# Performance work log

Measured on AMD Instinct MI355X. Metric: run time of the kernel, lower is better.

## Reference

```python
import jax, jax.numpy as jnp
import numpy as np

NODE_V = 16  # node_vocab_size
EDGE_V = 8   # edge_vocab_size
B, N = 64, 256


def _encode_single(x, vocab_size):
    # round to integer bucket, map bucket centers to (-1, 1)
    return 2.0 * ((jnp.round(x) + 0.5) / vocab_size) - 1.0


def setup_inputs() -> dict:
    key = jax.random.key(0)
    k1, k2, k3 = jax.random.split(key, 3)
    x_nodes = jax.random.uniform(k1, (B, N, 1), dtype=jnp.float32, minval=0.0, maxval=float(NODE_V))
    x_edges = jax.random.uniform(k2, (B, N, N), dtype=jnp.float32, minval=0.0, maxval=float(EDGE_V))
    g_0 = jax.random.normal(k3, (B,), dtype=jnp.float32)
    return {"x_nodes": x_nodes, "x_edges": x_edges, "g_0": g_0}


def reference(x_nodes, x_edges, g_0):
    # encode: quantize continuous inputs to bucket centers in (-1, 1)
    zn = _encode_single(x_nodes, NODE_V)  # [b, n, 1]
    ze = _encode_single(x_edges, EDGE_V)  # [b, n, n]

    # codebook values for each vocab bucket, also mapped to (-1, 1)
    node_vals = _encode_single(jnp.arange(NODE_V, dtype=jnp.float32), NODE_V)  # [Vn]
    edge_vals = _encode_single(jnp.arange(EDGE_V, dtype=jnp.float32), EDGE_V)  # [Ve]

    inv_stdev = jnp.exp(-0.5 * g_0)  # [b]

    # decode nodes: [b, n, 1] - [Vn] -> [b, n, Vn]
    node_logits = -0.5 * jnp.square((zn - node_vals) * inv_stdev[:, None, None])
    node_logprobs = jax.nn.log_softmax(node_logits, axis=-1)

    # decode edges: [b, n, n, 1] - [Ve] -> [b, n, n, Ve]
    edge_logits = -0.5 * jnp.square((ze[..., None] - edge_vals) * inv_stdev[:, None, None, None])
    edge_logprobs = jax.nn.log_softmax(edge_logits, axis=-1)

    return node_logprobs, edge_logprobs
```

## Files before the change

### kernel.cpp

```cpp
#include <hip/hip_runtime.h>
#include <hip/hip_bf16.h>

#define NODE_V 16
#define EDGE_V 8
#define BATCH  64
#define NSEQ   256

__global__ void node_kernel(const float* __restrict__ xn,
                            const float* __restrict__ g0,
                            float* __restrict__ out) {
    __shared__ __align__(16) float tbl[17 * 16];
    const int b = blockIdx.x;

    if (threadIdx.x < 17) {
        const float inv = __expf(-0.5f * g0[b]) ;
        const float inv_acc = expf(-0.5f * g0[b]);
        (void)inv;
        const int bucket = threadIdx.x;
        const float z = 2.0f * ((float)bucket + 0.5f) / (float)NODE_V - 1.0f;
        float l[NODE_V];
        float m = -1e30f;
        #pragma unroll
        for (int v = 0; v < NODE_V; ++v) {
            const float ev = 2.0f * ((float)v + 0.5f) / (float)NODE_V - 1.0f;
            const float d  = (z - ev) * inv_acc;
            l[v] = -0.5f * d * d;
            m = fmaxf(m, l[v]);
        }
        float s = 0.0f;
        #pragma unroll
        for (int v = 0; v < NODE_V; ++v) s += expf(l[v] - m);
        const float lse = m + logf(s);
        #pragma unroll
        for (int v = 0; v < NODE_V; ++v) tbl[bucket * NODE_V + v] = l[v] - lse;
    }
    __syncthreads();

    const int idx = b * NSEQ + threadIdx.x;
    const float x = xn[idx];
    const int bucket = (int)rintf(x);
    float4* o = (float4*)(out + (size_t)idx * NODE_V);
    const float4* t = (const float4*)&tbl[bucket * NODE_V];
    #pragma unroll
    for (int k = 0; k < 4; ++k) o[k] = t[k];
}

__global__ void edge_kernel(const float* __restrict__ xe,
                            const float* __restrict__ g0,
                            float* __restrict__ out) {
    __shared__ __align__(16) float tbl[9 * 8];
    const int b = blockIdx.y;

    if (threadIdx.x < 9) {
        const float inv = expf(-0.5f * g0[b]);
        const int bucket = threadIdx.x;
        const float z = 2.0f * ((float)bucket + 0.5f) / (float)EDGE_V - 1.0f;
        float l[EDGE_V];
        float m = -1e30f;
        #pragma unroll
        for (int v = 0; v < EDGE_V; ++v) {
            const float ev = 2.0f * ((float)v + 0.5f) / (float)EDGE_V - 1.0f;
            const float d  = (z - ev) * inv;
            l[v] = -0.5f * d * d;
            m = fmaxf(m, l[v]);
        }
        float s = 0.0f;
        #pragma unroll
        for (int v = 0; v < EDGE_V; ++v) s += expf(l[v] - m);
        const float lse = m + logf(s);
        #pragma unroll
        for (int v = 0; v < EDGE_V; ++v) tbl[bucket * EDGE_V + v] = l[v] - lse;
    }
    __syncthreads();

    const size_t idx = (size_t)b * (NSEQ * NSEQ) + (size_t)blockIdx.x * 256 + threadIdx.x;
    const float x = xe[idx];
    const int bucket = (int)rintf(x);
    const float4* t = (const float4*)&tbl[bucket * EDGE_V];
    float4* o = (float4*)(out + idx * EDGE_V);
    o[0] = t[0];
    o[1] = t[1];
}

extern "C" void kernel_launch(void* const* d_in, const int* in_sizes, int n_in,
                              void* d_out, int out_size, void* d_ws, size_t ws_size,
                              hipStream_t stream) {
    const float* xn = (const float*)d_in[0];
    const float* xe = (const float*)d_in[1];
    const float* g0 = (const float*)d_in[2];
    float* out = (float*)d_out;

    node_kernel<<<dim3(BATCH), dim3(NSEQ), 0, stream>>>(xn, g0, out);

    float* edge_out = out + (size_t)BATCH * NSEQ * NODE_V;
    edge_kernel<<<dim3(NSEQ * NSEQ / 256, BATCH), dim3(256), 0, stream>>>(xe, g0, edge_out);
}
```

Before: 34.02 us.

## Fuse node and edge kernels and coalesce output stores with float4 per thread

Merges the node and edge kernels into one launch, with the first blocks doing edges and the last 64 blocks doing nodes. Each thread now writes consecutive float4s across the block, so stores are fully coalesced rather than strided per element. Each edge block now covers 1024 elements in an 8-iteration loop. Shared tables are padded to strides of 12 and 20 floats to spread LDS banks. The cost is duplicate input loads (two threads read the same x) and fewer, larger blocks.

```diff
diff --git a/kernel.cpp b/kernel.cpp
--- a/kernel.cpp
+++ b/kernel.cpp
@@ -6,80 +6,88 @@
 #define BATCH  64
 #define NSEQ   256
 
-__global__ void node_kernel(const float* __restrict__ xn,
-                            const float* __restrict__ g0,
-                            float* __restrict__ out) {
-    __shared__ __align__(16) float tbl[17 * 16];
-    const int b = blockIdx.x;
+#define EDGE_ELEMS  (BATCH * NSEQ * NSEQ)
+#define EDGE_BLOCKS (EDGE_ELEMS / 1024)
+#define NODE_OUT_FLOATS ((size_t)BATCH * NSEQ * NODE_V)
 
-    if (threadIdx.x < 17) {
-        const float inv = __expf(-0.5f * g0[b]) ;
-        const float inv_acc = expf(-0.5f * g0[b]);
-        (void)inv;
-        const int bucket = threadIdx.x;
-        const float z = 2.0f * ((float)bucket + 0.5f) / (float)NODE_V - 1.0f;
-        float l[NODE_V];
-        float m = -1e30f;
+__global__ __launch_bounds__(256) void fused_kernel(const float* __restrict__ xn,
+                                                    const float* __restrict__ xe,
+                                                    const float* __restrict__ g0,
+                                                    float* __restrict__ out) {
+    if (blockIdx.x < EDGE_BLOCKS) {
+        __shared__ __align__(16) float tbl[9 * 12];
+        const int blk = blockIdx.x;
+        const int b   = blk >> 6;
+
+        if (threadIdx.x < 9) {
+            const float inv = expf(-0.5f * g0[b]);
+            const int bucket = threadIdx.x;
+            const float z = 2.0f * ((float)bucket + 0.5f) / (float)EDGE_V - 1.0f;
+            float l[EDGE_V];
+            float m = -1e30f;
+            #pragma unroll
+            for (int v = 0; v < EDGE_V; ++v) {
+                const float ev = 2.0f * ((float)v + 0.5f) / (float)EDGE_V - 1.0f;
+                const float d  = (z - ev) * inv;
+                l[v] = -0.5f * d * d;
+                m = fmaxf(m, l[v]);
+            }
+            float s = 0.0f;
+            #pragma unroll
+            for (int v = 0; v < EDGE_V; ++v) s += expf(l[v] - m);
+            const float lse = m + logf(s);
+            #pragma unroll
+            for (int v = 0; v < EDGE_V; ++v) tbl[bucket * 12 + v] = l[v] - lse;
+        }
+        __syncthreads();
+
+        const float4* t4 = (const float4*)tbl;
+        float4* o4 = (float4*)(out + NODE_OUT_FLOATS);
+        const size_t qbase = (size_t)blk * 2048;
         #pragma unroll
-        for (int v = 0; v < NODE_V; ++v) {
-            const float ev = 2.0f * ((float)v + 0.5f) / (float)NODE_V - 1.0f;
-            const float d  = (z - ev) * inv_acc;
-            l[v] = -0.5f * d * d;
-            m = fmaxf(m, l[v]);
+        for (int r = 0; r < 8; ++r) {
+            const size_t q = qbase + (size_t)(r * 256 + threadIdx.x);
+            const float x = xe[q >> 1];
+            const int bucket = (int)rintf(x);
+            o4[q] = t4[bucket * 3 + (int)(q & 1)];
         }
-        float s = 0.0f;
+    } else {
+        __shared__ __align__(16) float tbl[17 * 20];
+        const int b = blockIdx.x - EDGE_BLOCKS;
+
+        if (threadIdx.x < 17) {
+            const float inv = expf(-0.5f * g0[b]);
+            const int bucket = threadIdx.x;
+            const float z = 2.0f * ((float)bucket + 0.5f) / (float)NODE_V - 1.0f;
+            float l[NODE_V];
+            float m = -1e30f;
+            #pragma unroll
+            for (int v = 0; v < NODE_V; ++v) {
+                const float ev = 2.0f * ((float)v + 0.5f) / (float)NODE_V - 1.0f;
+                const float d  = (z - ev) * inv;
+                l[v] = -0.5f * d * d;
+                m = fmaxf(m, l[v]);
+            }
+            float s = 0.0f;
+            #pragma unroll
+            for (int v = 0; v < NODE_V; ++v) s += expf(l[v] - m);
+            const float lse = m + logf(s);
+            #pragma unroll
+            for (int v = 0; v < NODE_V; ++v) tbl[bucket * 20 + v] = l[v] - lse;
+        }
+        __syncthreads();
+
+        const float4* t4 = (const float4*)tbl;
+        float4* o4 = (float4*)out;
+        const size_t qbase = (size_t)b * 1024;
         #pragma unroll
-        for (int v = 0; v < NODE_V; ++v) s += expf(l[v] - m);
-        const float lse = m + logf(s);
-        #pragma unroll
-        for (int v = 0; v < NODE_V; ++v) tbl[bucket * NODE_V + v] = l[v] - lse;
+        for (int r = 0; r < 4; ++r) {
+            const int q = r * 256 + threadIdx.x;
+            const float x = xn[b * NSEQ + (q >> 2)];
+            const int bucket = (int)rintf(x);
+            o4[qbase + q] = t4[bucket * 5 + (q & 3)];
+        }
     }
-    __syncthreads();
-
-    const int idx = b * NSEQ + threadIdx.x;
-    const float x = xn[idx];
-    const int bucket = (int)rintf(x);
-    float4* o = (float4*)(out + (size_t)idx * NODE_V);
-    const float4* t = (const float4*)&tbl[bucket * NODE_V];
-    #pragma unroll
-    for (int k = 0; k < 4; ++k) o[k] = t[k];
-}
-
-__global__ void edge_kernel(const float* __restrict__ xe,
-                            const float* __restrict__ g0,
-                            float* __restrict__ out) {
-    __shared__ __align__(16) float tbl[9 * 8];
-    const int b = blockIdx.y;
-
-    if (threadIdx.x < 9) {
-        const float inv = expf(-0.5f * g0[b]);
-        const int bucket = threadIdx.x;
-        const float z = 2.0f * ((float)bucket + 0.5f) / (float)EDGE_V - 1.0f;
-        float l[EDGE_V];
-        float m = -1e30f;
-        #pragma unroll
-        for (int v = 0; v < EDGE_V; ++v) {
-            const float ev = 2.0f * ((float)v + 0.5f) / (float)EDGE_V - 1.0f;
-            const float d  = (z - ev) * inv;
-            l[v] = -0.5f * d * d;
-            m = fmaxf(m, l[v]);
-        }
-        float s = 0.0f;
-        #pragma unroll
-        for (int v = 0; v < EDGE_V; ++v) s += expf(l[v] - m);
-        const float lse = m + logf(s);
-        #pragma unroll
-        for (int v = 0; v < EDGE_V; ++v) tbl[bucket * EDGE_V + v] = l[v] - lse;
-    }
-    __syncthreads();
-
-    const size_t idx = (size_t)b * (NSEQ * NSEQ) + (size_t)blockIdx.x * 256 + threadIdx.x;
-    const float x = xe[idx];
-    const int bucket = (int)rintf(x);
-    const float4* t = (const float4*)&tbl[bucket * EDGE_V];
-    float4* o = (float4*)(out + idx * EDGE_V);
-    o[0] = t[0];
-    o[1] = t[1];
 }
 
 extern "C" void kernel_launch(void* const* d_in, const int* in_sizes, int n_in,
@@ -90,8 +98,5 @@
     const float* g0 = (const float*)d_in[2];
     float* out = (float*)d_out;
 
-    node_kernel<<<dim3(BATCH), dim3(NSEQ), 0, stream>>>(xn, g0, out);
-
-    float* edge_out = out + (size_t)BATCH * NSEQ * NODE_V;
-    edge_kernel<<<dim3(NSEQ * NSEQ / 256, BATCH), dim3(256), 0, stream>>>(xe, g0, edge_out);
+    fused_kernel<<<dim3(EDGE_BLOCKS + BATCH), dim3(256), 0, stream>>>(xn, xe, g0, out);
 }
```

After: 28.66 us. -15.8%, faster.
